# Optimization experiments

Hardware: AMD Instinct MI355X
Metric: run time of the kernel (lower is better)

Reference implementation:

```python
import jax, jax.numpy as jnp
import numpy as np

DIM = 4096
N_EXPERTS = 256
TOPK = 8
N_GROUPS = 8
TOPK_GROUPS = 4
ROUTE_SCALE = 2.5
N_TOKENS = 16384


def setup_inputs() -> dict:
    key = jax.random.key(0)
    k1, k2 = jax.random.split(key)
    x = jax.random.normal(k1, (N_TOKENS, DIM), dtype=jnp.float32)
    weight = jax.random.normal(k2, (N_EXPERTS, DIM), dtype=jnp.float32) * 0.01
    e_score_correction_bias = jnp.zeros((N_EXPERTS,), dtype=jnp.float32)
    return {"x": x, "weight": weight, "e_score_correction_bias": e_score_correction_bias}


def reference(x, weight, e_score_correction_bias):
    n = x.shape[0]
    # [n, E] expert scores
    scores = jax.nn.sigmoid(jnp.dot(x, weight.T))
    original_scores = scores
    scores = scores + e_score_correction_bias
    # group selection: top-2 sum per group -> top-k groups
    scores_g = scores.reshape(n, N_GROUPS, -1)  # [n, G, E/G]
    group_score = jnp.sort(scores_g, axis=-1)[..., -2:].sum(axis=-1)  # [n, G]
    group_idx = jnp.argsort(group_score, axis=-1)[..., -TOPK_GROUPS:]  # [n, kg]
    mask = jnp.ones((n, N_GROUPS), dtype=bool)
    mask = mask.at[jnp.arange(n)[:, None], group_idx].set(False)
    scores_masked = jnp.where(mask[..., None], -jnp.inf, scores_g).reshape(n, -1)
    # final top-k experts
    indices = jnp.argsort(scores_masked, axis=-1)[..., -TOPK:]  # [n, k]
    weights = original_scores[jnp.arange(n)[:, None], indices]  # [n, k]
    weights = weights / (weights.sum(axis=-1, keepdims=True) + 1e-20)
    weights = weights * ROUTE_SCALE
    return (weights, indices)
```

## Files before the change

kernel.cpp:

```cpp
#include <hip/hip_runtime.h>
#include <math.h>

#define DIMK 4096
#define NEXP 256
#define BM   32
#define BK32 32
#define NT128 (DIMK / BK32)
#define NGRP 8
#define GSZ  32
#define TOPKG 4
#define TOPKE 8
#define WS_NEED ((size_t)NT128 * 3 * 16 * 1024)

#define XPLANE 2048
#define XBUF   (3 * XPLANE)

typedef __bf16 bf16x8 __attribute__((ext_vector_type(8)));
typedef float f32x4 __attribute__((ext_vector_type(4)));

__device__ __forceinline__ int xslot(int token, int chunk) {
  return ((chunk * 32 + token) * 16) ^ ((token & 3) << 6);
}

__device__ __forceinline__ void decomp8(const float v[8], uint4& H, uint4& M, uint4& L) {
  union U { __bf16 b[8]; uint4 u; } h, m, l;
#pragma unroll
  for (int i = 0; i < 8; ++i) {
    float xv = v[i];
    __bf16 hb = (__bf16)xv;
    float r1 = xv - (float)hb;
    __bf16 mb = (__bf16)r1;
    float r2 = r1 - (float)mb;
    h.b[i] = hb; m.b[i] = mb; l.b[i] = (__bf16)r2;
  }
  H = h.u; M = m.u; L = l.u;
}

__global__ __launch_bounds__(256) void w_split_kernel(const float* __restrict__ wgt,
                                                      unsigned char* __restrict__ ws) {
  const int g = blockIdx.x * 256 + threadIdx.x;
  const int e = g >> 9;
  const int k0 = (g & 511) << 3;
  const int kt = k0 >> 5;
  const int chunk = (k0 & 31) >> 3;
  const int lane = chunk * 16 + (e & 15);
  const int eb = e >> 4;
  float v[8];
  float4 a = *(const float4*)(wgt + (long)e * DIMK + k0);
  float4 b = *(const float4*)(wgt + (long)e * DIMK + k0 + 4);
  v[0]=a.x; v[1]=a.y; v[2]=a.z; v[3]=a.w; v[4]=b.x; v[5]=b.y; v[6]=b.z; v[7]=b.w;
  uint4 H, M, L;
  decomp8(v, H, M, L);
  const long base = ((long)(kt * 3) * 16 + eb) * 1024 + lane * 16;
  *(uint4*)(ws + base)             = H;
  *(uint4*)(ws + base + 16 * 1024) = M;
  *(uint4*)(ws + base + 32 * 1024) = L;
}

__device__ __forceinline__ void mfma_group(const bf16x8 a[2], const bf16x8* b, f32x4 D[2][4]) {
#pragma unroll
  for (int rt = 0; rt < 2; ++rt)
#pragma unroll
    for (int ct = 0; ct < 4; ++ct)
      D[rt][ct] = __builtin_amdgcn_mfma_f32_16x16x32_bf16(a[rt], b[ct], D[rt][ct], 0, 0, 0);
}

__device__ __forceinline__ void groups_for_tile(const unsigned char* smem, int bufoff,
                                                int l15, int chunk, const bf16x8* B,
                                                f32x4 D[2][4]) {
  bf16x8 ah[2], am[2], al[2];
#pragma unroll
  for (int rt = 0; rt < 2; ++rt) {
    const int off = xslot(rt * 16 + l15, chunk);
    ah[rt] = *(const bf16x8*)(smem + bufoff + 0 * XPLANE + off);
    am[rt] = *(const bf16x8*)(smem + bufoff + 1 * XPLANE + off);
    al[rt] = *(const bf16x8*)(smem + bufoff + 2 * XPLANE + off);
  }
  mfma_group(ah, B + 0, D);
  mfma_group(am, B + 0, D);
  mfma_group(al, B + 0, D);
  mfma_group(ah, B + 4, D);
  mfma_group(am, B + 4, D);
  mfma_group(ah, B + 8, D);
}

__device__ __forceinline__ void loadB(bf16x8* dst, const unsigned char* ws, int t,
                                      int wid, int lane) {
#pragma unroll
  for (int p = 0; p < 3; ++p)
#pragma unroll
    for (int ct = 0; ct < 4; ++ct)
      dst[p * 4 + ct] = *(const bf16x8*)(ws + ((long)((t * 3 + p) * 16 + wid * 4 + ct) << 10) + lane * 16);
}

__global__ __launch_bounds__(256, 2) void moe_gate_mfma(
    const float* __restrict__ x, const unsigned char* __restrict__ ws,
    const float* __restrict__ bias, float* __restrict__ outw, float* __restrict__ outi) {
  __shared__ __align__(16) unsigned char smem[32 * 257 * 8];
  double* sc = (double*)smem;

  const int tid = threadIdx.x;
  const int wid = tid >> 6;
  const int lane = tid & 63;
  const int l15 = lane & 15;
  const int chunk = lane >> 4;
  const long bm0 = (long)blockIdx.x * BM;

  const int token = (tid >> 2) & 31;
  const int part = tid & 3;
  const bool stager = (tid < 128);
  const float* xptr = x + (bm0 + token) * (long)DIMK + part * 8;
  const int xw = xslot(token, part);

  f32x4 D[2][4];
  double acc[2][4][4];
#pragma unroll
  for (int rt = 0; rt < 2; ++rt)
#pragma unroll
    for (int ct = 0; ct < 4; ++ct) {
      D[rt][ct] = (f32x4){0.f, 0.f, 0.f, 0.f};
#pragma unroll
      for (int r = 0; r < 4; ++r) acc[rt][ct][r] = 0.0;
    }

  bf16x8 bA[12], bB[12];
  uint4 XH, XM, XL;

  loadB(bA, ws, 0, wid, lane);
  if (stager) {
    float v[8];
    float4 a0 = *(const float4*)(xptr);
    float4 a1 = *(const float4*)(xptr + 4);
    v[0]=a0.x; v[1]=a0.y; v[2]=a0.z; v[3]=a0.w; v[4]=a1.x; v[5]=a1.y; v[6]=a1.z; v[7]=a1.w;
    decomp8(v, XH, XM, XL);
    *(uint4*)(smem + 0 * XPLANE + xw) = XH;
    *(uint4*)(smem + 1 * XPLANE + xw) = XM;
    *(uint4*)(smem + 2 * XPLANE + xw) = XL;
  }
  __syncthreads();

#pragma unroll 1
  for (int it = 0; it < NT128 / 2; ++it) {
    const int t1 = 2 * it + 1;
    loadB(bB, ws, t1, wid, lane);
    if (stager) {
      float v[8];
      float4 a0 = *(const float4*)(xptr + t1 * BK32);
      float4 a1 = *(const float4*)(xptr + t1 * BK32 + 4);
      v[0]=a0.x; v[1]=a0.y; v[2]=a0.z; v[3]=a0.w; v[4]=a1.x; v[5]=a1.y; v[6]=a1.z; v[7]=a1.w;
      decomp8(v, XH, XM, XL);
    }
    groups_for_tile(smem, 0, l15, chunk, bA, D);
    if (stager) {
      *(uint4*)(smem + XBUF + 0 * XPLANE + xw) = XH;
      *(uint4*)(smem + XBUF + 1 * XPLANE + xw) = XM;
      *(uint4*)(smem + XBUF + 2 * XPLANE + xw) = XL;
    }
    __syncthreads();
    const bool more = (it + 1 < NT128 / 2);
    if (more) {
      loadB(bA, ws, t1 + 1, wid, lane);
      if (stager) {
        float v[8];
        float4 a0 = *(const float4*)(xptr + (t1 + 1) * BK32);
        float4 a1 = *(const float4*)(xptr + (t1 + 1) * BK32 + 4);
        v[0]=a0.x; v[1]=a0.y; v[2]=a0.z; v[3]=a0.w; v[4]=a1.x; v[5]=a1.y; v[6]=a1.z; v[7]=a1.w;
        decomp8(v, XH, XM, XL);
      }
    }
    groups_for_tile(smem, XBUF, l15, chunk, bB, D);
    if (more && stager) {
      *(uint4*)(smem + 0 * XPLANE + xw) = XH;
      *(uint4*)(smem + 1 * XPLANE + xw) = XM;
      *(uint4*)(smem + 2 * XPLANE + xw) = XL;
    }
    if ((it & 1) == 1) {
#pragma unroll
      for (int rt = 0; rt < 2; ++rt)
#pragma unroll
        for (int ct = 0; ct < 4; ++ct) {
#pragma unroll
          for (int r = 0; r < 4; ++r) acc[rt][ct][r] += (double)D[rt][ct][r];
          D[rt][ct] = (f32x4){0.f, 0.f, 0.f, 0.f};
        }
    }
    __syncthreads();
  }

#pragma unroll
  for (int rt = 0; rt < 2; ++rt)
#pragma unroll
    for (int ct = 0; ct < 4; ++ct) {
      const int col = wid * 64 + ct * 16 + l15;
      const double bd = (double)bias[col];
#pragma unroll
      for (int r = 0; r < 4; ++r) {
        const int row = rt * 16 + (lane >> 4) * 4 + r;
        const double s = 1.0 / (1.0 + exp(-acc[rt][ct][r]));
        sc[row * 257 + col] = s + bd;
      }
    }
  __syncthreads();

  if (tid < BM) {
    double* row = sc + tid * 257;
    double gs[NGRP];
#pragma unroll
    for (int g = 0; g < NGRP; ++g) {
      double m1 = -1e300, m2 = -1e300;
      for (int e = 0; e < GSZ; ++e) {
        double v = row[g * GSZ + e];
        if (v > m1) { m2 = m1; m1 = v; }
        else if (v > m2) { m2 = v; }
      }
      gs[g] = m1 + m2;
    }
    unsigned msk = 0;
#pragma unroll
    for (int g = 0; g < NGRP; ++g) {
      int cnt = 0;
#pragma unroll
      for (int h = 0; h < NGRP; ++h)
        cnt += ((gs[h] > gs[g]) || (gs[h] == gs[g] && h > g)) ? 1 : 0;
      if (cnt < TOPKG) msk |= (1u << g);
    }
    int g0 = __ffs(msk) - 1; msk &= msk - 1;
    int g1 = __ffs(msk) - 1; msk &= msk - 1;
    int g2 = __ffs(msk) - 1; msk &= msk - 1;
    int g3 = __ffs(msk) - 1;

    double wv[TOPKE];
    float iv[TOPKE];
#pragma unroll
    for (int r8 = 0; r8 < TOPKE; ++r8) {
      double best = -1e300;
      int bi = 0;
      {
        int gg = g0;
        for (int e = 0; e < GSZ; ++e) { double v = row[gg * GSZ + e]; if (v >= best) { best = v; bi = gg * GSZ + e; } }
        gg = g1;
        for (int e = 0; e < GSZ; ++e) { double v = row[gg * GSZ + e]; if (v >= best) { best = v; bi = gg * GSZ + e; } }
        gg = g2;
        for (int e = 0; e < GSZ; ++e) { double v = row[gg * GSZ + e]; if (v >= best) { best = v; bi = gg * GSZ + e; } }
        gg = g3;
        for (int e = 0; e < GSZ; ++e) { double v = row[gg * GSZ + e]; if (v >= best) { best = v; bi = gg * GSZ + e; } }
      }
      row[bi] = -1e300;
      wv[7 - r8] = best - (double)bias[bi];
      iv[7 - r8] = (float)bi;
    }
    double sum = 0.0;
#pragma unroll
    for (int p = 0; p < TOPKE; ++p) sum += wv[p];
    const double den = sum + 1e-20;
    const long trow = bm0 + tid;
#pragma unroll
    for (int p = 0; p < TOPKE; ++p) {
      outw[trow * 8 + p] = (float)(wv[p] / den * 2.5);
      outi[trow * 8 + p] = iv[p];
    }
  }
}

#define BMF  64
#define BKF 16
#define LXSF 68
__global__ __launch_bounds__(256, 1) void moe_gate_f64(
    const float* __restrict__ x, const float* __restrict__ wgt,
    const float* __restrict__ bias, float* __restrict__ outw,
    float* __restrict__ outi) {
  __shared__ __align__(16) unsigned char smem[64 * 257 * 8];
  float* lw = (float*)smem;
  float* lx = (float*)(smem + 32768);
  double* sc = (double*)smem;
  const int tid = threadIdx.x;
  const long bm0 = (long)blockIdx.x * BMF;
  const int rg = tid >> 5;
  const int cg = tid & 31;
  const int sxr = tid >> 2;
  const int sxj = (tid & 3) << 2;
  const float* xrow = x + (bm0 + sxr) * (long)DIMK + sxj;
  const float* wrow = wgt + (long)tid * DIMK;
  double acc[8][8];
#pragma unroll
  for (int i = 0; i < 8; ++i)
#pragma unroll
    for (int j = 0; j < 8; ++j) acc[i][j] = 0.0;
#define LWF(b, k, e) lw[((b)*BKF + (k)) * NEXP + (e)]
#define LXF(b, k, r) lx[((b)*BKF + (k)) * LXSF + (r)]
  {
    float4 xv = *(const float4*)(xrow);
#pragma unroll
    for (int c = 0; c < 4; ++c) LXF(0, sxj + c, sxr) = ((const float*)&xv)[c];
#pragma unroll
    for (int jj = 0; jj < 4; ++jj) {
      float4 wv = *(const float4*)(wrow + jj * 4);
#pragma unroll
      for (int c = 0; c < 4; ++c) LWF(0, jj * 4 + c, tid) = ((const float*)&wv)[c];
    }
  }
  __syncthreads();
  const int NTF = DIMK / BKF;
  for (int kt = 0; kt < NTF; ++kt) {
    const int b = kt & 1;
    if (kt + 1 < NTF) {
      const int k0 = (kt + 1) * BKF;
      const int nb = b ^ 1;
      float4 xv = *(const float4*)(xrow + k0);
      float4 wv0 = *(const float4*)(wrow + k0);
      float4 wv1 = *(const float4*)(wrow + k0 + 4);
      float4 wv2 = *(const float4*)(wrow + k0 + 8);
      float4 wv3 = *(const float4*)(wrow + k0 + 12);
#pragma unroll
      for (int c = 0; c < 4; ++c) LXF(nb, sxj + c, sxr) = ((const float*)&xv)[c];
#pragma unroll
      for (int c = 0; c < 4; ++c) LWF(nb, 0 + c, tid) = ((const float*)&wv0)[c];
#pragma unroll
      for (int c = 0; c < 4; ++c) LWF(nb, 4 + c, tid) = ((const float*)&wv1)[c];
#pragma unroll
      for (int c = 0; c < 4; ++c) LWF(nb, 8 + c, tid) = ((const float*)&wv2)[c];
#pragma unroll
      for (int c = 0; c < 4; ++c) LWF(nb, 12 + c, tid) = ((const float*)&wv3)[c];
    }
#pragma unroll
    for (int k = 0; k < BKF; ++k) {
      float4 a0 = *(const float4*)(&LXF(b, k, rg * 8));
      float4 a1 = *(const float4*)(&LXF(b, k, rg * 8 + 4));
      double ad[8] = {(double)a0.x, (double)a0.y, (double)a0.z, (double)a0.w,
                      (double)a1.x, (double)a1.y, (double)a1.z, (double)a1.w};
      double bd[8];
#pragma unroll
      for (int j = 0; j < 4; ++j) {
        float2 bb = *(const float2*)(&LWF(b, k, cg * 2 + 64 * j));
        bd[2 * j] = (double)bb.x;
        bd[2 * j + 1] = (double)bb.y;
      }
#pragma unroll
      for (int i = 0; i < 8; ++i)
#pragma unroll
        for (int j = 0; j < 8; ++j) acc[i][j] += ad[i] * bd[j];
    }
    __syncthreads();
  }
  double bc[8];
#pragma unroll
  for (int j = 0; j < 4; ++j) {
    bc[2 * j] = (double)bias[cg * 2 + 64 * j];
    bc[2 * j + 1] = (double)bias[cg * 2 + 64 * j + 1];
  }
#pragma unroll
  for (int i = 0; i < 8; ++i) {
    const int r = rg * 8 + i;
#pragma unroll
    for (int jq = 0; jq < 8; ++jq) {
      const int col = cg * 2 + 64 * (jq >> 1) + (jq & 1);
      double s = 1.0 / (1.0 + exp(-acc[i][jq]));
      sc[r * 257 + col] = s + bc[jq];
    }
  }
  __syncthreads();
  if (tid < BMF) {
    double* row = sc + tid * 257;
    double gs[NGRP];
#pragma unroll
    for (int g = 0; g < NGRP; ++g) {
      double m1 = -1e300, m2 = -1e300;
      for (int e = 0; e < GSZ; ++e) {
        double v = row[g * GSZ + e];
        if (v > m1) { m2 = m1; m1 = v; }
        else if (v > m2) { m2 = v; }
      }
      gs[g] = m1 + m2;
    }
    unsigned msk = 0;
#pragma unroll
    for (int g = 0; g < NGRP; ++g) {
      int cnt = 0;
#pragma unroll
      for (int h = 0; h < NGRP; ++h)
        cnt += ((gs[h] > gs[g]) || (gs[h] == gs[g] && h > g)) ? 1 : 0;
      if (cnt < TOPKG) msk |= (1u << g);
    }
    int g0 = __ffs(msk) - 1; msk &= msk - 1;
    int g1 = __ffs(msk) - 1; msk &= msk - 1;
    int g2 = __ffs(msk) - 1; msk &= msk - 1;
    int g3 = __ffs(msk) - 1;
    double wv[TOPKE];
    float iv[TOPKE];
#pragma unroll
    for (int r8 = 0; r8 < TOPKE; ++r8) {
      double best = -1e300;
      int bi = 0;
      {
        int gg = g0;
        for (int e = 0; e < GSZ; ++e) { double v = row[gg * GSZ + e]; if (v >= best) { best = v; bi = gg * GSZ + e; } }
        gg = g1;
        for (int e = 0; e < GSZ; ++e) { double v = row[gg * GSZ + e]; if (v >= best) { best = v; bi = gg * GSZ + e; } }
        gg = g2;
        for (int e = 0; e < GSZ; ++e) { double v = row[gg * GSZ + e]; if (v >= best) { best = v; bi = gg * GSZ + e; } }
        gg = g3;
        for (int e = 0; e < GSZ; ++e) { double v = row[gg * GSZ + e]; if (v >= best) { best = v; bi = gg * GSZ + e; } }
      }
      row[bi] = -1e300;
      wv[7 - r8] = best - (double)bias[bi];
      iv[7 - r8] = (float)bi;
    }
    double sum = 0.0;
#pragma unroll
    for (int p = 0; p < TOPKE; ++p) sum += wv[p];
    const double den = sum + 1e-20;
    const long trow = bm0 + tid;
#pragma unroll
    for (int p = 0; p < TOPKE; ++p) {
      outw[trow * 8 + p] = (float)(wv[p] / den * 2.5);
      outi[trow * 8 + p] = iv[p];
    }
  }
}

extern "C" void kernel_launch(void* const* d_in, const int* in_sizes, int n_in,
                              void* d_out, int out_size, void* d_ws, size_t ws_size,
                              hipStream_t stream) {
  const float* x = (const float*)d_in[0];
  const float* w = (const float*)d_in[1];
  const float* b = (const float*)d_in[2];
  const int ntok = in_sizes[0] / DIMK;
  float* outw = (float*)d_out;
  float* outi = outw + (size_t)ntok * 8;
  if (ws_size >= WS_NEED) {
    hipLaunchKernelGGL(w_split_kernel, dim3(512), dim3(256), 0, stream,
                       w, (unsigned char*)d_ws);
    hipLaunchKernelGGL(moe_gate_mfma, dim3(ntok / BM), dim3(256), 0, stream,
                       x, (const unsigned char*)d_ws, b, outw, outi);
  } else {
    hipLaunchKernelGGL(moe_gate_f64, dim3(ntok / 64), dim3(256), 0, stream,
                       x, w, b, outw, outi);
  }
}
```

Before: 282.0 us.

## Stage expert weight tiles in LDS and double the token tile to 64

The token tile grows from 32 to 64 rows and the block from 4 to 8 waves in a 2x4 wave grid. The pre-split bf16 weight tiles are now loaded cooperatively into double-buffered LDS, so each weight tile is shared across 64 tokens. Before, every wave read its weight fragments straight from global memory for only 32 tokens. The loop now processes one K tile per iteration with an LDS double buffer and raises wave priority around the MFMA section. LDS use grows to about 128 KB per block, which likely allows only one block per CU.

```diff
diff --git a/kernel.cpp b/kernel.cpp
--- a/kernel.cpp
+++ b/kernel.cpp
@@ -3,30 +3,44 @@
 
 #define DIMK 4096
 #define NEXP 256
-#define BM   32
+#define BM   64
 #define BK32 32
-#define NT128 (DIMK / BK32)
+#define NT   (DIMK / BK32)
 #define NGRP 8
 #define GSZ  32
 #define TOPKG 4
 #define TOPKE 8
-#define WS_NEED ((size_t)NT128 * 3 * 16 * 1024)
-
-#define XPLANE 2048
-#define XBUF   (3 * XPLANE)
+#define WS_NEED ((size_t)NT * 3 * 16 * 1024)
+
+#define LDSB_OFF 0
+#define BTILE    49152
+#define LDSX_OFF 98304
+#define XTILE    12288
+#define SMEM_SZ  131584
 
 typedef __bf16 bf16x8 __attribute__((ext_vector_type(8)));
 typedef float f32x4 __attribute__((ext_vector_type(4)));
 
-__device__ __forceinline__ int xslot(int token, int chunk) {
-  return ((chunk * 32 + token) * 16) ^ ((token & 3) << 6);
-}
-
 __device__ __forceinline__ void decomp8(const float v[8], uint4& H, uint4& M, uint4& L) {
   union U { __bf16 b[8]; uint4 u; } h, m, l;
 #pragma unroll
   for (int i = 0; i < 8; ++i) {
     float xv = v[i];
+    __bf16 hb = (__bf16)xv;
+    float r1 = xv - (float)hb;
+    __bf16 mb = (__bf16)r1;
+    float r2 = r1 - (float)mb;
+    h.b[i] = hb; m.b[i] = mb; l.b[i] = (__bf16)r2;
+  }
+  H = h.u; M = m.u; L = l.u;
+}
+
+__device__ __forceinline__ void decomp4(float4 v, uint2& H, uint2& M, uint2& L) {
+  union U { __bf16 b[4]; uint2 u; } h, m, l;
+  float vv[4] = {v.x, v.y, v.z, v.w};
+#pragma unroll
+  for (int i = 0; i < 4; ++i) {
+    float xv = vv[i];
     __bf16 hb = (__bf16)xv;
     float r1 = xv - (float)hb;
     __bf16 mb = (__bf16)r1;
@@ -57,7 +71,7 @@
   *(uint4*)(ws + base + 32 * 1024) = L;
 }
 
-__device__ __forceinline__ void mfma_group(const bf16x8 a[2], const bf16x8* b, f32x4 D[2][4]) {
+__device__ __forceinline__ void mfma_group(const bf16x8 a[2], const bf16x8 b[4], f32x4 D[2][4]) {
 #pragma unroll
   for (int rt = 0; rt < 2; ++rt)
 #pragma unroll
@@ -65,52 +79,26 @@
       D[rt][ct] = __builtin_amdgcn_mfma_f32_16x16x32_bf16(a[rt], b[ct], D[rt][ct], 0, 0, 0);
 }
 
-__device__ __forceinline__ void groups_for_tile(const unsigned char* smem, int bufoff,
-                                                int l15, int chunk, const bf16x8* B,
-                                                f32x4 D[2][4]) {
-  bf16x8 ah[2], am[2], al[2];
-#pragma unroll
-  for (int rt = 0; rt < 2; ++rt) {
-    const int off = xslot(rt * 16 + l15, chunk);
-    ah[rt] = *(const bf16x8*)(smem + bufoff + 0 * XPLANE + off);
-    am[rt] = *(const bf16x8*)(smem + bufoff + 1 * XPLANE + off);
-    al[rt] = *(const bf16x8*)(smem + bufoff + 2 * XPLANE + off);
-  }
-  mfma_group(ah, B + 0, D);
-  mfma_group(am, B + 0, D);
-  mfma_group(al, B + 0, D);
-  mfma_group(ah, B + 4, D);
-  mfma_group(am, B + 4, D);
-  mfma_group(ah, B + 8, D);
-}
-
-__device__ __forceinline__ void loadB(bf16x8* dst, const unsigned char* ws, int t,
-                                      int wid, int lane) {
-#pragma unroll
-  for (int p = 0; p < 3; ++p)
-#pragma unroll
-    for (int ct = 0; ct < 4; ++ct)
-      dst[p * 4 + ct] = *(const bf16x8*)(ws + ((long)((t * 3 + p) * 16 + wid * 4 + ct) << 10) + lane * 16);
-}
-
-__global__ __launch_bounds__(256, 2) void moe_gate_mfma(
+__global__ __launch_bounds__(512, 2) void moe_gate_mfma(
     const float* __restrict__ x, const unsigned char* __restrict__ ws,
     const float* __restrict__ bias, float* __restrict__ outw, float* __restrict__ outi) {
-  __shared__ __align__(16) unsigned char smem[32 * 257 * 8];
+  __shared__ __align__(16) unsigned char smem[SMEM_SZ];
   double* sc = (double*)smem;
 
   const int tid = threadIdx.x;
-  const int wid = tid >> 6;
   const int lane = tid & 63;
   const int l15 = lane & 15;
-  const int chunk = lane >> 4;
+  const int wid = tid >> 6;
+  const int wr = wid >> 2;
+  const int wc = wid & 3;
   const long bm0 = (long)blockIdx.x * BM;
 
-  const int token = (tid >> 2) & 31;
-  const int part = tid & 3;
-  const bool stager = (tid < 128);
-  const float* xptr = x + (bm0 + token) * (long)DIMK + part * 8;
-  const int xw = xslot(token, part);
+  const int xtok = tid >> 3;
+  const int xq = tid & 7;
+  const float* xptr = x + (bm0 + xtok) * (long)DIMK + xq * 4;
+  const int xwoff = LDSX_OFF + (xq >> 1) * 1024 + xtok * 16 + (xq & 1) * 8;
+
+  const unsigned char* wsp = ws + tid * 16;
 
   f32x4 D[2][4];
   double acc[2][4][4];
@@ -123,58 +111,72 @@
       for (int r = 0; r < 4; ++r) acc[rt][ct][r] = 0.0;
     }
 
-  bf16x8 bA[12], bB[12];
-  uint4 XH, XM, XL;
-
-  loadB(bA, ws, 0, wid, lane);
-  if (stager) {
-    float v[8];
-    float4 a0 = *(const float4*)(xptr);
-    float4 a1 = *(const float4*)(xptr + 4);
-    v[0]=a0.x; v[1]=a0.y; v[2]=a0.z; v[3]=a0.w; v[4]=a1.x; v[5]=a1.y; v[6]=a1.z; v[7]=a1.w;
-    decomp8(v, XH, XM, XL);
-    *(uint4*)(smem + 0 * XPLANE + xw) = XH;
-    *(uint4*)(smem + 1 * XPLANE + xw) = XM;
-    *(uint4*)(smem + 2 * XPLANE + xw) = XL;
+  float4 xv;
+  uint4 bs[6];
+
+  xv = *(const float4*)(xptr);
+#pragma unroll
+  for (int j = 0; j < 6; ++j) bs[j] = *(const uint4*)(wsp + j * 8192);
+  {
+    uint2 H, M, L;
+    decomp4(xv, H, M, L);
+    *(uint2*)(smem + xwoff + 0 * 4096) = H;
+    *(uint2*)(smem + xwoff + 1 * 4096) = M;
+    *(uint2*)(smem + xwoff + 2 * 4096) = L;
+#pragma unroll
+    for (int j = 0; j < 6; ++j)
+      *(uint4*)(smem + LDSB_OFF + j * 8192 + tid * 16) = bs[j];
   }
   __syncthreads();
 
 #pragma unroll 1
-  for (int it = 0; it < NT128 / 2; ++it) {
-    const int t1 = 2 * it + 1;
-    loadB(bB, ws, t1, wid, lane);
-    if (stager) {
-      float v[8];
-      float4 a0 = *(const float4*)(xptr + t1 * BK32);
-      float4 a1 = *(const float4*)(xptr + t1 * BK32 + 4);
-      v[0]=a0.x; v[1]=a0.y; v[2]=a0.z; v[3]=a0.w; v[4]=a1.x; v[5]=a1.y; v[6]=a1.z; v[7]=a1.w;
-      decomp8(v, XH, XM, XL);
-    }
-    groups_for_tile(smem, 0, l15, chunk, bA, D);
-    if (stager) {
-      *(uint4*)(smem + XBUF + 0 * XPLANE + xw) = XH;
-      *(uint4*)(smem + XBUF + 1 * XPLANE + xw) = XM;
-      *(uint4*)(smem + XBUF + 2 * XPLANE + xw) = XL;
-    }
-    __syncthreads();
-    const bool more = (it + 1 < NT128 / 2);
+  for (int t = 0; t < NT; ++t) {
+    const int buf = t & 1, nbuf = buf ^ 1;
+    const bool more = (t + 1 < NT);
     if (more) {
-      loadB(bA, ws, t1 + 1, wid, lane);
-      if (stager) {
-        float v[8];
-        float4 a0 = *(const float4*)(xptr + (t1 + 1) * BK32);
-        float4 a1 = *(const float4*)(xptr + (t1 + 1) * BK32 + 4);
-        v[0]=a0.x; v[1]=a0.y; v[2]=a0.z; v[3]=a0.w; v[4]=a1.x; v[5]=a1.y; v[6]=a1.z; v[7]=a1.w;
-        decomp8(v, XH, XM, XL);
-      }
-    }
-    groups_for_tile(smem, XBUF, l15, chunk, bB, D);
-    if (more && stager) {
-      *(uint4*)(smem + 0 * XPLANE + xw) = XH;
-      *(uint4*)(smem + 1 * XPLANE + xw) = XM;
-      *(uint4*)(smem + 2 * XPLANE + xw) = XL;
-    }
-    if ((it & 1) == 1) {
+      xv = *(const float4*)(xptr + (t + 1) * BK32);
+      const unsigned char* wst = wsp + (long)(t + 1) * BTILE;
+#pragma unroll
+      for (int j = 0; j < 6; ++j) bs[j] = *(const uint4*)(wst + j * 8192);
+    }
+    const unsigned char* xb = smem + LDSX_OFF + buf * XTILE;
+    const unsigned char* bb = smem + LDSB_OFF + buf * BTILE;
+    bf16x8 ah[2], am[2], al[2];
+#pragma unroll
+    for (int rt = 0; rt < 2; ++rt) {
+      const int ao = (lane >> 4) * 1024 + (wr * 32 + rt * 16 + l15) * 16;
+      ah[rt] = *(const bf16x8*)(xb + 0 * 4096 + ao);
+      am[rt] = *(const bf16x8*)(xb + 1 * 4096 + ao);
+      al[rt] = *(const bf16x8*)(xb + 2 * 4096 + ao);
+    }
+    bf16x8 bh[4], bmm[4], bl[4];
+#pragma unroll
+    for (int ct = 0; ct < 4; ++ct) {
+      const int bo = (wc * 4 + ct) * 1024 + lane * 16;
+      bh[ct]  = *(const bf16x8*)(bb + 0 * 16384 + bo);
+      bmm[ct] = *(const bf16x8*)(bb + 1 * 16384 + bo);
+      bl[ct]  = *(const bf16x8*)(bb + 2 * 16384 + bo);
+    }
+    __builtin_amdgcn_s_setprio(1);
+    mfma_group(ah, bh, D);
+    mfma_group(am, bh, D);
+    mfma_group(al, bh, D);
+    mfma_group(ah, bmm, D);
+    mfma_group(am, bmm, D);
+    mfma_group(ah, bl, D);
+    __builtin_amdgcn_s_setprio(0);
+    if (more) {
+      uint2 H, M, L;
+      decomp4(xv, H, M, L);
+      unsigned char* xw = smem + xwoff + nbuf * XTILE;
+      *(uint2*)(xw + 0 * 4096) = H;
+      *(uint2*)(xw + 1 * 4096) = M;
+      *(uint2*)(xw + 2 * 4096) = L;
+      unsigned char* bw = smem + LDSB_OFF + nbuf * BTILE + tid * 16;
+#pragma unroll
+      for (int j = 0; j < 6; ++j) *(uint4*)(bw + j * 8192) = bs[j];
+    }
+    if (t & 1) {
 #pragma unroll
       for (int rt = 0; rt < 2; ++rt)
 #pragma unroll
@@ -191,11 +193,11 @@
   for (int rt = 0; rt < 2; ++rt)
 #pragma unroll
     for (int ct = 0; ct < 4; ++ct) {
-      const int col = wid * 64 + ct * 16 + l15;
+      const int col = wc * 64 + ct * 16 + l15;
       const double bd = (double)bias[col];
 #pragma unroll
       for (int r = 0; r < 4; ++r) {
-        const int row = rt * 16 + (lane >> 4) * 4 + r;
+        const int row = wr * 32 + rt * 16 + (lane >> 4) * 4 + r;
         const double s = 1.0 / (1.0 + exp(-acc[rt][ct][r]));
         sc[row * 257 + col] = s + bd;
       }
@@ -430,7 +432,7 @@
   if (ws_size >= WS_NEED) {
     hipLaunchKernelGGL(w_split_kernel, dim3(512), dim3(256), 0, stream,
                        w, (unsigned char*)d_ws);
-    hipLaunchKernelGGL(moe_gate_mfma, dim3(ntok / BM), dim3(256), 0, stream,
+    hipLaunchKernelGGL(moe_gate_mfma, dim3(ntok / BM), dim3(512), 0, stream,
                        x, (const unsigned char*)d_ws, b, outw, outi);
   } else {
     hipLaunchKernelGGL(moe_gate_f64, dim3(ntok / 64), dim3(256), 0, stream,
```

Result: slower. 502.9 us (+78.3%).
